# Kernel optimization log

Hardware: AMD Instinct MI355X
Metric: run time of the kernel (lower is better)

Reference implementation:

```python
import jax, jax.numpy as jnp
import numpy as np

EPS = 1e-5

def rmsnorm(x, w):
    return x * jax.lax.rsqrt(jnp.mean(x * x, axis=-1, keepdims=True) + EPS) * w

def silu(x):
    return x * jax.nn.sigmoid(x)

def causal_conv1d(x, w, b):
    # x: (B, L, D); w: (D, K) depthwise causal conv; b: (D,)
    B, L, D = x.shape
    K = w.shape[-1]
    xt = jnp.transpose(x, (0, 2, 1))  # (B, D, L)
    out = jax.lax.conv_general_dilated(
        xt, w[:, None, :], window_strides=(1,), padding=[(K - 1, 0)],
        feature_group_count=D, dimension_numbers=('NCH', 'OIH', 'NCH'))
    return jnp.transpose(out + b[None, :, None], (0, 2, 1))

def selective_scan(u, dt, A, Bm, Cm, Dp):
    # u, dt: (B,L,Di); A: (Di,S); Bm, Cm: (B,L,S); Dp: (Di,)
    dA = jnp.exp(dt[..., None] * A)                    # (B,L,Di,S)
    dBu = (dt * u)[..., None] * Bm[:, :, None, :]      # (B,L,Di,S)
    def step(h, inp):
        dA_t, dBu_t, C_t = inp
        h = dA_t * h + dBu_t
        y = jnp.einsum('bds,bs->bd', h, C_t)
        return h, y
    h0 = jnp.zeros((dA.shape[0],) + dA.shape[2:], dA.dtype)
    _, ys = jax.lax.scan(step, h0,
                         (dA.transpose(1, 0, 2, 3), dBu.transpose(1, 0, 2, 3), Cm.transpose(1, 0, 2)))
    return ys.transpose(1, 0, 2) + u * Dp

def mamba_inner(x, z, cw, cb, xpw, dpw, dpb, A_log, Dp, dt_rank, d_state):
    x = silu(causal_conv1d(x, cw, cb))
    x_dbl = jnp.einsum('bld,ed->ble', x, xpw)
    dt_r, Bm, Cm = jnp.split(x_dbl, [dt_rank, dt_rank + d_state], axis=-1)
    dt = jax.nn.softplus(jnp.einsum('blr,dr->bld', dt_r, dpw) + dpb)
    y = selective_scan(x, dt, -jnp.exp(A_log), Bm, Cm, Dp)
    return y * silu(z)

def setup_inputs() -> dict:
    key = jax.random.key(0)
    B, C, T, H, W = 2, 3, 4, 224, 224
    E, P, depth, n_spa = 384, 16, 12, 6
    Di, S, R, K = 2 * E, 8, (E + 15) // 16, 4
    N = (H // P) * (W // P)
    ks = iter(jax.random.split(key, 64))
    nrm = lambda shape, std=0.02: jax.random.normal(next(ks), shape, jnp.float32) * std
    A_init = jnp.log(jnp.tile(jnp.arange(1, S + 1, dtype=jnp.float32), (Di, 1)))
    inp = {
        'x': jax.random.normal(next(ks), (B, C, T, H, W), jnp.float32),
        'patch_w': nrm((E, C, 1, P, P)),
        'patch_b': jnp.zeros((E,), jnp.float32),
        'pos_embed': nrm((1, N, E)),
        'in_proj_w': nrm((depth, 2 * Di, E)),
        'conv_w': nrm((depth, Di, K), 0.2),
        'conv_b': jnp.zeros((depth, Di), jnp.float32),
        'xproj_w': nrm((depth, R + 2 * S, Di)),
        'dtproj_w': nrm((depth, Di, R), R ** -0.5),
        'dtproj_b': jnp.full((depth, Di), -4.0, jnp.float32) + nrm((depth, Di), 0.1),
        'A_log': jnp.tile(A_init[None], (depth, 1, 1)),
        'D_param': jnp.ones((depth, Di), jnp.float32),
        'outproj_w': nrm((depth, E, Di)),
        'norm_w': jnp.ones((depth, E), jnp.float32),
        'conv_wb': nrm((n_spa, Di, K), 0.2),
        'conv_bb': jnp.zeros((n_spa, Di), jnp.float32),
        'xproj_wb': nrm((n_spa, R + 2 * S, Di)),
        'dtproj_wb': nrm((n_spa, Di, R), R ** -0.5),
        'dtproj_bb': jnp.full((n_spa, Di), -4.0, jnp.float32) + nrm((n_spa, Di), 0.1),
        'A_log_b': jnp.tile(A_init[None], (n_spa, 1, 1)),
        'D_b': jnp.ones((n_spa, Di), jnp.float32),
        'norm_f_w': jnp.ones((E,), jnp.float32),
    }
    return inp

def reference(x, patch_w, patch_b, pos_embed, in_proj_w, conv_w, conv_b, xproj_w,
              dtproj_w, dtproj_b, A_log, D_param, outproj_w, norm_w,
              conv_wb, conv_bb, xproj_wb, dtproj_wb, dtproj_bb, A_log_b, D_b,
              norm_f_w):
    B, C, T, H, W = x.shape
    E = patch_w.shape[0]
    P = patch_w.shape[-1]
    Hp, Wp = H // P, W // P
    N = Hp * Wp
    # patch embed: Conv3d, kernel = stride = (1, P, P)
    xp = x.reshape(B, C, T, Hp, P, Wp, P)
    tok = jnp.einsum('bcthpwq,ecpq->bthwe', xp, patch_w[:, :, 0]) + patch_b
    tok = tok.reshape(B, T, N, E) + pos_embed[:, None]
    # sinusoidal temporal positional encoding
    pos = jnp.arange(T, dtype=jnp.float32)[:, None]
    div = jnp.exp(-jnp.log(10000.0) * jnp.arange(0, E, 2, dtype=jnp.float32) / E)
    pe = jnp.zeros((T, E), jnp.float32)
    pe = pe.at[:, 0::2].set(jnp.sin(pos * div)).at[:, 1::2].set(jnp.cos(pos * div))
    h = (tok + pe[None, :, None, :]).reshape(B, T * N, E)

    depth = in_proj_w.shape[0]
    n_spa = conv_wb.shape[0]
    Di = conv_w.shape[1]
    S = A_log.shape[-1]
    R = dtproj_w.shape[-1]
    residual = None
    for i in range(depth):
        residual = h if residual is None else h + residual
        hn = rmsnorm(residual, norm_w[i])
        xz = jnp.einsum('ble,fe->blf', hn, in_proj_w[i])
        xm, z = xz[..., :Di], xz[..., Di:]
        y = mamba_inner(xm, z, conv_w[i], conv_b[i], xproj_w[i],
                        dtproj_w[i], dtproj_b[i], A_log[i], D_param[i], R, S)
        if i < n_spa:  # bimamba: scan reversed sequence with backward params
            yb = mamba_inner(xm[:, ::-1], z[:, ::-1], conv_wb[i], conv_bb[i], xproj_wb[i],
                             dtproj_wb[i], dtproj_bb[i], A_log_b[i], D_b[i], R, S)
            y = y + yb[:, ::-1]
        h = jnp.einsum('bli,ei->ble', y, outproj_w[i])
    residual = h + residual
    return rmsnorm(residual, norm_f_w)
```

## Files before the change

### kernel.cpp

```cpp
#include <hip/hip_runtime.h>
#include <hip/hip_bf16.h>
#include <math.h>

#define Bn   2
#define Tn   4
#define Nn   196
#define Ln   784
#define Mn   1568
#define En   384
#define Din  768
#define Sn   8
#define Rn   24
#define DEPTH 12
#define NSPA 6
#define NC   98
#define CL   8

typedef __attribute__((ext_vector_type(8))) short bf16x8;
typedef __attribute__((ext_vector_type(4))) float f32x4;

__device__ __forceinline__ float siluf(float v) { return v / (1.f + __expf(-v)); }
__device__ __forceinline__ float us2f(unsigned short u) {
    union { unsigned int i; float f; } v; v.i = (unsigned)u << 16; return v.f;
}
__device__ __forceinline__ unsigned short f2us(float f) {
    __hip_bfloat16 b = __float2bfloat16(f);
    return *(unsigned short*)&b;
}
__device__ __forceinline__ void cstore(float* p, float v) { *p = v; }
__device__ __forceinline__ void cstore(unsigned short* p, float v) { *p = f2us(v); }

__device__ __forceinline__ void xcd_tile(int ny, int& n0, int& m0)
{
    int nx = gridDim.x;
    int total = nx*ny;
    int bid = blockIdx.y*nx + blockIdx.x;
    int q = total >> 3, r = total & 7;
    int xcd = bid & 7, idx = bid >> 3;
    int base = (xcd < r) ? xcd*(q+1) : r*(q+1) + (xcd - r)*q;
    int flat = base + idx;
    n0 = (flat / ny) * 64;
    m0 = (flat % ny) * 64;
}

#define NW0 7077888
#define NW1 3538944
#define NW2 368640
#define NW3 184320
#define NW4 294912
__device__ __forceinline__ void cast4(unsigned short* d, const float* s)
{
    float4 v = *(const float4*)s;
    ushort4 o;
    o.x = f2us(v.x); o.y = f2us(v.y); o.z = f2us(v.z); o.w = f2us(v.w);
    *(ushort4*)d = o;
}
__global__ __launch_bounds__(256) void k_castw(
    const float* __restrict__ w0, const float* __restrict__ w1,
    const float* __restrict__ w2, const float* __restrict__ w3,
    const float* __restrict__ w4,
    unsigned short* __restrict__ o0, unsigned short* __restrict__ o1,
    unsigned short* __restrict__ o2, unsigned short* __restrict__ o3,
    unsigned short* __restrict__ o4)
{
    int i4 = (blockIdx.x*blockDim.x + threadIdx.x)*4;
    if (i4 < NW0) { cast4(o0+i4, w0+i4); return; }
    i4 -= NW0;
    if (i4 < NW1) { cast4(o1+i4, w1+i4); return; }
    i4 -= NW1;
    if (i4 < NW2) { cast4(o2+i4, w2+i4); return; }
    i4 -= NW2;
    if (i4 < NW3) { cast4(o3+i4, w3+i4); return; }
    i4 -= NW3;
    if (i4 < NW4) { cast4(o4+i4, w4+i4); }
}

__global__ __launch_bounds__(256) void k_patch(
    const float* __restrict__ x, unsigned short* __restrict__ pm)
{
    int gid = blockIdx.x*blockDim.x + threadIdx.x;
    if (gid >= Mn*768) return;
    int idx = gid % 768, token = gid / 768;
    int b = token / Ln, l = token % Ln;
    int t = l / Nn, n = l % Nn;
    int hh = n / 14, ww = n % 14;
    int c = idx >> 8, rem = idx & 255, p = rem >> 4, q = rem & 15;
    pm[gid] = f2us(x[(((size_t)(b*3 + c)*Tn + t)*224 + (hh*16 + p))*224 + (ww*16 + q)]);
}

__global__ __launch_bounds__(256) void k_posadd(
    float* __restrict__ h, const float* __restrict__ pb,
    const float* __restrict__ pos)
{
    int gid = blockIdx.x*blockDim.x + threadIdx.x;
    if (gid >= Mn*En) return;
    int e = gid % En, token = gid / En;
    int l = token % Ln;
    int t = l / Nn, n = l % Nn;
    float div = __expf(-logf(10000.f) * (float)(e & ~1) / (float)En);
    float ang = (float)t * div;
    h[gid] += pb[e] + pos[n*En + e] + ((e & 1) ? cosf(ang) : sinf(ang));
}

__global__ __launch_bounds__(256) void rms_residual(
    const float* __restrict__ hin, float* __restrict__ res,
    unsigned short* __restrict__ hn, const float* __restrict__ w, int first)
{
    int wid  = (blockIdx.x * blockDim.x + threadIdx.x) >> 6;
    int lane = threadIdx.x & 63;
    if (wid >= Mn) return;
    const float* hp = hin + (size_t)wid*En;
    float* rp = res + (size_t)wid*En;
    float v[6]; float ss = 0.f;
    #pragma unroll
    for (int j = 0; j < 6; ++j) {
        int e = lane + j*64;
        float r = first ? hp[e] : (hp[e] + rp[e]);
        v[j] = r; ss = fmaf(r, r, ss);
    }
    #pragma unroll
    for (int off = 32; off; off >>= 1) ss += __shfl_xor(ss, off, 64);
    float scale = rsqrtf(ss * (1.f/(float)En) + 1e-5f);
    #pragma unroll
    for (int j = 0; j < 6; ++j) {
        int e = lane + j*64;
        rp[e] = v[j];
        hn[(size_t)wid*En + e] = f2us(v[j] * scale * w[e]);
    }
}

template<typename CT, int GATED>
__global__ __launch_bounds__(256) void gemm_mfma(
    const unsigned short* __restrict__ A,
    const unsigned short* __restrict__ Yb,
    const unsigned short* __restrict__ Z,
    const unsigned short* __restrict__ Wb,
    CT* __restrict__ C, int ldc, int M, int N, int K, int ndir)
{
    __shared__ unsigned short As[2][64][72];
    __shared__ unsigned short Bs[2][64][72];
    int n0, m0;
    xcd_tile((M + 63) >> 6, n0, m0);
    int tid = threadIdx.x;
    int wave = tid >> 6, lane = tid & 63;
    int quad = lane >> 4, fr = lane & 15;
    int arow = tid >> 2;
    int c8   = (tid & 3) << 3;
    int mg = m0 + arow; if (mg >= M) mg = M - 1;
    f32x4 acc[4] = {};

    auto gate8 = [&](const unsigned short* yf, const unsigned short* yb,
                     const unsigned short* zp) -> bf16x8 {
        bf16x8 f = *(const bf16x8*)yf;
        bf16x8 bb = *(const bf16x8*)yb;
        bf16x8 zz = *(const bf16x8*)zp;
        unsigned short o[8];
        const unsigned short* fu = (const unsigned short*)&f;
        const unsigned short* bu = (const unsigned short*)&bb;
        const unsigned short* zu = (const unsigned short*)&zz;
        #pragma unroll
        for (int j = 0; j < 8; ++j) {
            float v = us2f(fu[j]);
            if (ndir == 2) v += us2f(bu[j]);
            o[j] = f2us(v * siluf(us2f(zu[j])));
        }
        return *(bf16x8*)o;
    };

    auto load_tile = [&](int k0, bf16x8& av0, bf16x8& av1,
                         bf16x8& wv0, bf16x8& wv1) {
        if (!GATED) {
            av0 = *(const bf16x8*)(A + (size_t)mg*K + k0 + c8);
            av1 = *(const bf16x8*)(A + (size_t)mg*K + k0 + c8 + 32);
        } else {
            size_t ro = (size_t)mg*K + k0 + c8;
            size_t zo = (size_t)mg*1536 + k0 + c8;
            av0 = gate8(A + ro, Yb + ro, Z + zo);
            av1 = gate8(A + ro + 32, Yb + ro + 32, Z + zo + 32);
        }
        wv0 = *(const bf16x8*)(Wb + (size_t)(n0 + arow)*K + k0 + c8);
        wv1 = *(const bf16x8*)(Wb + (size_t)(n0 + arow)*K + k0 + c8 + 32);
    };

    {
        bf16x8 a0, a1, w0, w1;
        load_tile(0, a0, a1, w0, w1);
        *(bf16x8*)&As[0][arow][c8]      = a0;
        *(bf16x8*)&As[0][arow][c8 + 32] = a1;
        *(bf16x8*)&Bs[0][arow][c8]      = w0;
        *(bf16x8*)&Bs[0][arow][c8 + 32] = w1;
    }
    int cur = 0;
    for (int k0 = 64; k0 <= K; k0 += 64) {
        bool more = (k0 < K);
        bf16x8 a0, a1, w0, w1;
        if (more) load_tile(k0, a0, a1, w0, w1);
        __syncthreads();
        bf16x8 af0 = *(const bf16x8*)&As[cur][wave*16 + fr][quad << 3];
        bf16x8 af1 = *(const bf16x8*)&As[cur][wave*16 + fr][(quad << 3) + 32];
        #pragma unroll
        for (int nt = 0; nt < 4; ++nt) {
            bf16x8 b0 = *(const bf16x8*)&Bs[cur][nt*16 + fr][quad << 3];
            bf16x8 b1 = *(const bf16x8*)&Bs[cur][nt*16 + fr][(quad << 3) + 32];
            acc[nt] = __builtin_amdgcn_mfma_f32_16x16x32_bf16(af0, b0, acc[nt], 0, 0, 0);
            acc[nt] = __builtin_amdgcn_mfma_f32_16x16x32_bf16(af1, b1, acc[nt], 0, 0, 0);
        }
        if (more) {
            *(bf16x8*)&As[cur^1][arow][c8]      = a0;
            *(bf16x8*)&As[cur^1][arow][c8 + 32] = a1;
            *(bf16x8*)&Bs[cur^1][arow][c8]      = w0;
            *(bf16x8*)&Bs[cur^1][arow][c8 + 32] = w1;
            cur ^= 1;
        }
    }
    #pragma unroll
    for (int nt = 0; nt < 4; ++nt) {
        #pragma unroll
        for (int r = 0; r < 4; ++r) {
            int mgo = m0 + wave*16 + quad*4 + r;
            if (mgo < M) cstore(C + (size_t)mgo*ldc + n0 + nt*16 + fr, acc[nt][r]);
        }
    }
}

__global__ __launch_bounds__(256) void k_conv2(
    const unsigned short* __restrict__ xz,
    const float* __restrict__ cwf, const float* __restrict__ cbf,
    const float* __restrict__ cwb, const float* __restrict__ cbb,
    unsigned short* __restrict__ u, int ndir)
{
    int gid = blockIdx.x*blockDim.x + threadIdx.x;
    if (gid >= ndir*Mn*Din) return;
    int dir = gid / (Mn*Din);
    int rem = gid % (Mn*Din);
    int d = rem % Din, m = rem / Din;
    int l = m % Ln, b = m / Ln;
    const float* cw = dir ? cwb : cwf;
    const float* cb = dir ? cbb : cbf;
    float4 cwv = *(const float4*)(cw + d*4);
    float acc = cb[d];
    #pragma unroll
    for (int k = 0; k < 4; ++k) {
        int ls = l - 3 + k;
        if (ls < 0) continue;
        int lsrc = dir ? (Ln - 1 - ls) : ls;
        float cwk = (k==0)?cwv.x:(k==1)?cwv.y:(k==2)?cwv.z:cwv.w;
        acc = fmaf(us2f(xz[(size_t)(b*Ln + lsrc)*1536 + d]), cwk, acc);
    }
    u[gid] = f2us(siluf(acc));
}

__global__ __launch_bounds__(256) void xproj_gemm(
    const unsigned short* __restrict__ u,
    const unsigned short* __restrict__ xwf, const unsigned short* __restrict__ xwb,
    float* __restrict__ xd)
{
    __shared__ unsigned short As[2][64][72];
    __shared__ unsigned short Bs[2][64][72];
    int n0d, m0;
    xcd_tile((Mn + 63) >> 6, n0d, m0);
    int dir = n0d >> 6;
    const unsigned short* A = u + (size_t)dir*Mn*Din;
    const unsigned short* W = dir ? xwb : xwf;
    float* C = xd + (size_t)dir*Mn*40;
    int tid = threadIdx.x;
    int wave = tid >> 6, lane = tid & 63;
    int quad = lane >> 4, fr = lane & 15;
    int arow = tid >> 2;
    int c8   = (tid & 3) << 3;
    int mg = m0 + arow; if (mg >= Mn) mg = Mn - 1;
    int wrow = arow < 40 ? arow : 39;
    f32x4 acc[4] = {};

    auto load_tile = [&](int k0, bf16x8& av0, bf16x8& av1,
                         bf16x8& wv0, bf16x8& wv1) {
        av0 = *(const bf16x8*)(A + (size_t)mg*Din + k0 + c8);
        av1 = *(const bf16x8*)(A + (size_t)mg*Din + k0 + c8 + 32);
        wv0 = *(const bf16x8*)(W + (size_t)wrow*Din + k0 + c8);
        wv1 = *(const bf16x8*)(W + (size_t)wrow*Din + k0 + c8 + 32);
    };

    {
        bf16x8 a0, a1, w0, w1;
        load_tile(0, a0, a1, w0, w1);
        *(bf16x8*)&As[0][arow][c8]      = a0;
        *(bf16x8*)&As[0][arow][c8 + 32] = a1;
        *(bf16x8*)&Bs[0][arow][c8]      = w0;
        *(bf16x8*)&Bs[0][arow][c8 + 32] = w1;
    }
    int cur = 0;
    for (int k0 = 64; k0 <= Din; k0 += 64) {
        bool more = (k0 < Din);
        bf16x8 a0, a1, w0, w1;
        if (more) load_tile(k0, a0, a1, w0, w1);
        __syncthreads();
        bf16x8 af0 = *(const bf16x8*)&As[cur][wave*16 + fr][quad << 3];
        bf16x8 af1 = *(const bf16x8*)&As[cur][wave*16 + fr][(quad << 3) + 32];
        #pragma unroll
        for (int nt = 0; nt < 4; ++nt) {
            bf16x8 b0 = *(const bf16x8*)&Bs[cur][nt*16 + fr][quad << 3];
            bf16x8 b1 = *(const bf16x8*)&Bs[cur][nt*16 + fr][(quad << 3) + 32];
            acc[nt] = __builtin_amdgcn_mfma_f32_16x16x32_bf16(af0, b0, acc[nt], 0, 0, 0);
            acc[nt] = __builtin_amdgcn_mfma_f32_16x16x32_bf16(af1, b1, acc[nt], 0, 0, 0);
        }
        if (more) {
            *(bf16x8*)&As[cur^1][arow][c8]      = a0;
            *(bf16x8*)&As[cur^1][arow][c8 + 32] = a1;
            *(bf16x8*)&Bs[cur^1][arow][c8]      = w0;
            *(bf16x8*)&Bs[cur^1][arow][c8 + 32] = w1;
            cur ^= 1;
        }
    }
    #pragma unroll
    for (int nt = 0; nt < 4; ++nt) {
        int col = nt*16 + fr;
        if (col >= 40) continue;
        #pragma unroll
        for (int r = 0; r < 4; ++r) {
            int mgo = m0 + wave*16 + quad*4 + r;
            if (mgo < Mn) C[(size_t)mgo*40 + col] = acc[nt][r];
        }
    }
}

__global__ __launch_bounds__(256) void scanA(
    const unsigned short* __restrict__ u, const float* __restrict__ xd,
    const float* __restrict__ dwf, const float* __restrict__ dbf,
    const float* __restrict__ dwb, const float* __restrict__ dbb,
    const float* __restrict__ Alf, const float* __restrict__ Alb,
    float* __restrict__ Hsum, float* __restrict__ dtsum, int ndir)
{
    int gid = blockIdx.x*blockDim.x + threadIdx.x;
    if (gid >= ndir*Bn*NC*Din) return;
    int dir = gid / (Bn*NC*Din);
    int rem = gid % (Bn*NC*Din);
    int d = rem % Din;
    int bc = rem / Din;
    int c = bc % NC, b = bc / NC;
    const float* A_log = dir ? Alb : Alf;
    const float* dw = dir ? dwb : dwf;
    const float* db = dir ? dbb : dbf;
    float A[Sn];
    #pragma unroll
    for (int s = 0; s < Sn; ++s) A[s] = -__expf(A_log[d*Sn + s]);
    float dwr[Rn];
    #pragma unroll
    for (int r = 0; r < Rn; ++r) dwr[r] = dw[d*Rn + r];
    float dbv = db[d];
    float hs[Sn] = {0,0,0,0,0,0,0,0};
    float sdt = 0.f;
    int l0 = c*CL;
    const unsigned short* up = u + (size_t)dir*Mn*Din + ((size_t)b*Ln + l0)*Din + d;
    const float* xp = xd + (size_t)dir*Mn*40 + ((size_t)b*Ln + l0)*40;
    #pragma unroll
    for (int l = 0; l < CL; ++l) {
        float uv = us2f(up[(size_t)l*Din]);
        const float* xr = xp + l*40;
        float dta = dbv;
        #pragma unroll
        for (int r = 0; r < Rn; ++r) dta = fmaf(xr[r], dwr[r], dta);
        float dtv = (dta > 20.f) ? dta : log1pf(__expf(dta));
        sdt += dtv;
        const float4* B4 = (const float4*)(xr + Rn);
        float4 Bv0 = B4[0], Bv1 = B4[1];
        float du = dtv * uv;
        hs[0] = fmaf(__expf(dtv*A[0]), hs[0], du*Bv0.x);
        hs[1] = fmaf(__expf(dtv*A[1]), hs[1], du*Bv0.y);
        hs[2] = fmaf(__expf(dtv*A[2]), hs[2], du*Bv0.z);
        hs[3] = fmaf(__expf(dtv*A[3]), hs[3], du*Bv0.w);
        hs[4] = fmaf(__expf(dtv*A[4]), hs[4], du*Bv1.x);
        hs[5] = fmaf(__expf(dtv*A[5]), hs[5], du*Bv1.y);
        hs[6] = fmaf(__expf(dtv*A[6]), hs[6], du*Bv1.z);
        hs[7] = fmaf(__expf(dtv*A[7]), hs[7], du*Bv1.w);
    }
    float4* Hp = (float4*)(Hsum + (size_t)gid*8);
    Hp[0] = make_float4(hs[0], hs[1], hs[2], hs[3]);
    Hp[1] = make_float4(hs[4], hs[5], hs[6], hs[7]);
    dtsum[gid] = sdt;
}

__global__ __launch_bounds__(256) void scanB(
    const float* __restrict__ Alf, const float* __restrict__ Alb,
    float* __restrict__ Hsum, const float* __restrict__ dtsum, int ndir)
{
    int gid = blockIdx.x*blockDim.x + threadIdx.x;
    if (gid >= ndir*Bn*Din*Sn) return;
    int s   = gid & 7;
    int rem = gid >> 3;
    int d   = rem % Din;
    int t   = rem / Din;
    int b   = t % Bn, dir = t / Bn;
    const float* A_log = dir ? Alb : Alf;
    float Av = -__expf(A_log[d*Sn + s]);
    float h = 0.f;
    size_t base = (size_t)dir*Bn*NC*Din + (size_t)b*NC*Din + d;
    float* Hp = Hsum + base*8 + s;
    const float* dp = dtsum + base;
    #pragma unroll 7
    for (int c = 0; c < NC; ++c) {
        size_t off = (size_t)c*Din;
        float H = Hp[off*8];
        float sdt = dp[off];
        Hp[off*8] = h;
        h = fmaf(__expf(Av*sdt), h, H);
    }
}

__global__ __launch_bounds__(256) void scanC(
    const unsigned short* __restrict__ u, const float* __restrict__ xd,
    const float* __restrict__ dwf, const float* __restrict__ dbf,
    const float* __restrict__ dwb, const float* __restrict__ dbb,
    const float* __restrict__ Alf, const float* __restrict__ Alb,
    const float* __restrict__ Dpf, const float* __restrict__ Dpb,
    const float* __restrict__ Hsum, unsigned short* __restrict__ yt, int ndir)
{
    int gid = blockIdx.x*blockDim.x + threadIdx.x;
    if (gid >= ndir*Bn*NC*Din) return;
    int dir = gid / (Bn*NC*Din);
    int rem = gid % (Bn*NC*Din);
    int d = rem % Din;
    int bc = rem / Din;
    int c = bc % NC, b = bc / NC;
    const float* A_log = dir ? Alb : Alf;
    const float* dw = dir ? dwb : dwf;
    const float* db = dir ? dbb : dbf;
    const float* Dp = dir ? Dpb : Dpf;
    float A[Sn];
    #pragma unroll
    for (int s = 0; s < Sn; ++s) A[s] = -__expf(A_log[d*Sn + s]);
    float dwr[Rn];
    #pragma unroll
    for (int r = 0; r < Rn; ++r) dwr[r] = dw[d*Rn + r];
    float dbv = db[d];
    const float4* hp = (const float4*)(Hsum + (size_t)gid*8);
    float4 h0 = hp[0], h1 = hp[1];
    float hs[Sn] = {h0.x, h0.y, h0.z, h0.w, h1.x, h1.y, h1.z, h1.w};
    float Dd = Dp[d];
    int l0 = c*CL;
    const unsigned short* up = u + (size_t)dir*Mn*Din + ((size_t)b*Ln + l0)*Din + d;
    const float* xp = xd + (size_t)dir*Mn*40 + ((size_t)b*Ln + l0)*40;
    unsigned short* yp = yt + (size_t)dir*Mn*Din + (size_t)b*Ln*Din + d;
    #pragma unroll
    for (int l = 0; l < CL; ++l) {
        int gl = l0 + l;
        float uv = us2f(up[(size_t)l*Din]);
        const float* xr = xp + l*40;
        float dta = dbv;
        #pragma unroll
        for (int r = 0; r < Rn; ++r) dta = fmaf(xr[r], dwr[r], dta);
        float dtv = (dta > 20.f) ? dta : log1pf(__expf(dta));
        const float4* B4 = (const float4*)(xr + Rn);
        float4 Bv0 = B4[0], Bv1 = B4[1], Cv0 = B4[2], Cv1 = B4[3];
        float du = dtv * uv;
        float yv = 0.f;
        hs[0] = fmaf(__expf(dtv*A[0]), hs[0], du*Bv0.x); yv = fmaf(hs[0], Cv0.x, yv);
        hs[1] = fmaf(__expf(dtv*A[1]), hs[1], du*Bv0.y); yv = fmaf(hs[1], Cv0.y, yv);
        hs[2] = fmaf(__expf(dtv*A[2]), hs[2], du*Bv0.z); yv = fmaf(hs[2], Cv0.z, yv);
        hs[3] = fmaf(__expf(dtv*A[3]), hs[3], du*Bv0.w); yv = fmaf(hs[3], Cv0.w, yv);
        hs[4] = fmaf(__expf(dtv*A[4]), hs[4], du*Bv1.x); yv = fmaf(hs[4], Cv1.x, yv);
        hs[5] = fmaf(__expf(dtv*A[5]), hs[5], du*Bv1.y); yv = fmaf(hs[5], Cv1.y, yv);
        hs[6] = fmaf(__expf(dtv*A[6]), hs[6], du*Bv1.z); yv = fmaf(hs[6], Cv1.z, yv);
        hs[7] = fmaf(__expf(dtv*A[7]), hs[7], du*Bv1.w); yv = fmaf(hs[7], Cv1.w, yv);
        yv = fmaf(uv, Dd, yv);
        int ol = dir ? (Ln - 1 - gl) : gl;
        yp[(size_t)ol*Din] = f2us(yv);
    }
}

__global__ __launch_bounds__(256) void final_k(
    const float* __restrict__ h, const float* __restrict__ res,
    const float* __restrict__ w, float* __restrict__ out)
{
    int wid  = (blockIdx.x * blockDim.x + threadIdx.x) >> 6;
    int lane = threadIdx.x & 63;
    if (wid >= Mn) return;
    const float* hp = h + (size_t)wid*En;
    const float* rp = res + (size_t)wid*En;
    float v[6]; float ss = 0.f;
    #pragma unroll
    for (int j = 0; j < 6; ++j) {
        int e = lane + j*64;
        float r = hp[e] + rp[e];
        v[j] = r; ss = fmaf(r, r, ss);
    }
    #pragma unroll
    for (int off = 32; off; off >>= 1) ss += __shfl_xor(ss, off, 64);
    float scale = rsqrtf(ss * (1.f/(float)En) + 1e-5f);
    #pragma unroll
    for (int j = 0; j < 6; ++j) {
        int e = lane + j*64;
        out[(size_t)wid*En + e] = v[j] * scale * w[e];
    }
}

extern "C" void kernel_launch(void* const* d_in, const int* in_sizes, int n_in,
                              void* d_out, int out_size, void* d_ws, size_t ws_size,
                              hipStream_t stream)
{
    const float* x         = (const float*)d_in[0];
    const float* patch_w   = (const float*)d_in[1];
    const float* patch_b   = (const float*)d_in[2];
    const float* pos_embed = (const float*)d_in[3];
    const float* in_proj_w = (const float*)d_in[4];
    const float* conv_w    = (const float*)d_in[5];
    const float* conv_b    = (const float*)d_in[6];
    const float* xproj_w   = (const float*)d_in[7];
    const float* dtproj_w  = (const float*)d_in[8];
    const float* dtproj_b  = (const float*)d_in[9];
    const float* A_log     = (const float*)d_in[10];
    const float* D_param   = (const float*)d_in[11];
    const float* outproj_w = (const float*)d_in[12];
    const float* norm_w    = (const float*)d_in[13];
    const float* conv_wb   = (const float*)d_in[14];
    const float* conv_bb   = (const float*)d_in[15];
    const float* xproj_wb  = (const float*)d_in[16];
    const float* dtproj_wb = (const float*)d_in[17];
    const float* dtproj_bb = (const float*)d_in[18];
    const float* A_log_b   = (const float*)d_in[19];
    const float* D_b       = (const float*)d_in[20];
    const float* norm_f_w  = (const float*)d_in[21];

    float* pf   = (float*)d_ws;
    float* h    = pf;  pf += (size_t)Mn*En;
    float* res  = pf;  pf += (size_t)Mn*En;
    float* xd   = pf;  pf += (size_t)2*Mn*40;
    float* Hsum = pf;  pf += (size_t)2*Bn*NC*Din*Sn;
    float* dtsm = pf;  pf += (size_t)2*Bn*NC*Din;
    unsigned short* ub = (unsigned short*)pf;
    unsigned short* xz = ub;  ub += (size_t)Mn*1536;
    unsigned short* u  = ub;  ub += (size_t)2*Mn*Din;
    unsigned short* hn = u;
    unsigned short* yt = ub;  ub += (size_t)2*Mn*Din;
    unsigned short* w_in = ub;  ub += (size_t)NW0;
    unsigned short* w_out= ub;  ub += (size_t)NW1;
    unsigned short* w_xf = ub;  ub += (size_t)NW2;
    unsigned short* w_xb = ub;  ub += (size_t)NW3;
    unsigned short* w_pm = ub;  ub += (size_t)NW4;
    unsigned short* pm = (unsigned short*)Hsum;
    size_t needed = (size_t)((char*)ub - (char*)d_ws);
    if (ws_size < needed) return;

    const int wave_blocks = (Mn*64)/256;
    const int B_me   = (Mn*En + 255)/256;
    const int B_md   = (Mn*768 + 255)/256;
    const int B_cw   = ((NW0+NW1+NW2+NW3+NW4)/4 + 255)/256;
    const int mTiles = (Mn + 63)/64;

    k_castw<<<B_cw, 256, 0, stream>>>(in_proj_w, outproj_w, xproj_w, xproj_wb,
                                      patch_w, w_in, w_out, w_xf, w_xb, w_pm);
    k_patch<<<B_md, 256, 0, stream>>>(x, pm);
    dim3 g0(En/64, mTiles);
    gemm_mfma<float,0><<<g0, 256, 0, stream>>>(pm, nullptr, nullptr, w_pm,
                                               h, En, Mn, En, 768, 1);
    k_posadd<<<B_me, 256, 0, stream>>>(h, patch_b, pos_embed);

    for (int i = 0; i < DEPTH; ++i) {
        int ndir = (i < NSPA) ? 2 : 1;
        rms_residual<<<wave_blocks, 256, 0, stream>>>(h, res, hn, norm_w + (size_t)i*En, i == 0);

        dim3 g1(1536/64, mTiles);
        gemm_mfma<unsigned short,0><<<g1, 256, 0, stream>>>(
            hn, nullptr, nullptr, w_in + (size_t)i*1536*En,
            xz, 1536, Mn, 1536, En, 1);

        const float* cwf = conv_w + (size_t)i*Din*4;
        const float* cbf = conv_b + (size_t)i*Din;
        const float* dwf = dtproj_w + (size_t)i*Din*Rn;
        const float* dbf = dtproj_b + (size_t)i*Din;
        const float* Alf = A_log + (size_t)i*Din*Sn;
        const float* Dpf = D_param + (size_t)i*Din;
        const float* cwb = conv_wb + (size_t)i*Din*4;
        const float* cbb = conv_bb + (size_t)i*Din;
        const float* dwb = dtproj_wb + (size_t)i*Din*Rn;
        const float* dbb = dtproj_bb + (size_t)i*Din;
        const float* Alb = A_log_b + (size_t)i*Din*Sn;
        const float* Dpb = D_b + (size_t)i*Din;
        const unsigned short* xwf = w_xf + (size_t)i*40*Din;
        const unsigned short* xwb = w_xb + (size_t)i*40*Din;

        int c_blocks  = (ndir*Mn*Din + 255)/256;
        int sA_blocks = (ndir*Bn*NC*Din + 255)/256;
        int sB_blocks = (ndir*Bn*Din*Sn + 255)/256;

        k_conv2<<<c_blocks, 256, 0, stream>>>(xz, cwf, cbf, cwb, cbb, u, ndir);
        dim3 gx(ndir, mTiles);
        xproj_gemm<<<gx, 256, 0, stream>>>(u, xwf, xwb, xd);
        scanA<<<sA_blocks, 256, 0, stream>>>(u, xd, dwf, dbf, dwb, dbb,
                                             Alf, Alb, Hsum, dtsm, ndir);
        scanB<<<sB_blocks, 256, 0, stream>>>(Alf, Alb, Hsum, dtsm, ndir);
        scanC<<<sA_blocks, 256, 0, stream>>>(u, xd, dwf, dbf, dwb, dbb,
                                             Alf, Alb, Dpf, Dpb, Hsum, yt, ndir);

        dim3 g2(En/64, mTiles);
        gemm_mfma<float,1><<<g2, 256, 0, stream>>>(
            yt, yt + (size_t)Mn*Din, xz + Din, w_out + (size_t)i*En*Din,
            h, En, Mn, En, Din, ndir);
    }

    final_k<<<wave_blocks, 256, 0, stream>>>(h, res, norm_f_w, (float*)d_out);
}
```

Before: 1.261 ms.

## Split-K the narrow GEMMs into two partial buffers and fuse conv into xproj

```diff
diff --git a/kernel.cpp b/kernel.cpp
--- a/kernel.cpp
+++ b/kernel.cpp
@@ -89,8 +89,8 @@
 }
 
 __global__ __launch_bounds__(256) void k_posadd(
-    float* __restrict__ h, const float* __restrict__ pb,
-    const float* __restrict__ pos)
+    float* __restrict__ h, const float* __restrict__ h2,
+    const float* __restrict__ pb, const float* __restrict__ pos)
 {
     int gid = blockIdx.x*blockDim.x + threadIdx.x;
     if (gid >= Mn*En) return;
@@ -99,23 +99,25 @@
     int t = l / Nn, n = l % Nn;
     float div = __expf(-logf(10000.f) * (float)(e & ~1) / (float)En);
     float ang = (float)t * div;
-    h[gid] += pb[e] + pos[n*En + e] + ((e & 1) ? cosf(ang) : sinf(ang));
+    h[gid] += h2[gid] + pb[e] + pos[n*En + e] + ((e & 1) ? cosf(ang) : sinf(ang));
 }
 
 __global__ __launch_bounds__(256) void rms_residual(
-    const float* __restrict__ hin, float* __restrict__ res,
-    unsigned short* __restrict__ hn, const float* __restrict__ w, int first)
+    const float* __restrict__ hin, const float* __restrict__ h2,
+    float* __restrict__ res, unsigned short* __restrict__ hn,
+    const float* __restrict__ w, int first)
 {
     int wid  = (blockIdx.x * blockDim.x + threadIdx.x) >> 6;
     int lane = threadIdx.x & 63;
     if (wid >= Mn) return;
     const float* hp = hin + (size_t)wid*En;
+    const float* h2p = h2 + (size_t)wid*En;
     float* rp = res + (size_t)wid*En;
     float v[6]; float ss = 0.f;
     #pragma unroll
     for (int j = 0; j < 6; ++j) {
         int e = lane + j*64;
-        float r = first ? hp[e] : (hp[e] + rp[e]);
+        float r = first ? hp[e] : (hp[e] + h2p[e] + rp[e]);
         v[j] = r; ss = fmaf(r, r, ss);
     }
     #pragma unroll
@@ -129,7 +131,7 @@
     }
 }
 
-template<typename CT, int GATED>
+template<typename CT, int GATED, int SK>
 __global__ __launch_bounds__(256) void gemm_mfma(
     const unsigned short* __restrict__ A,
     const unsigned short* __restrict__ Yb,
@@ -141,6 +143,12 @@
     __shared__ unsigned short Bs[2][64][72];
     int n0, m0;
     xcd_tile((M + 63) >> 6, n0, m0);
+    int nidx = n0 >> 6;
+    int zk = nidx % SK;
+    n0 = (nidx / SK) * 64;
+    int kbeg = zk * (K / SK);
+    int kend = kbeg + K / SK;
+    CT* Cz = C + (size_t)zk*M*ldc;
     int tid = threadIdx.x;
     int wave = tid >> 6, lane = tid & 63;
     int quad = lane >> 4, fr = lane & 15;
@@ -184,15 +192,15 @@
 
     {
         bf16x8 a0, a1, w0, w1;
-        load_tile(0, a0, a1, w0, w1);
+        load_tile(kbeg, a0, a1, w0, w1);
         *(bf16x8*)&As[0][arow][c8]      = a0;
         *(bf16x8*)&As[0][arow][c8 + 32] = a1;
         *(bf16x8*)&Bs[0][arow][c8]      = w0;
         *(bf16x8*)&Bs[0][arow][c8 + 32] = w1;
     }
     int cur = 0;
-    for (int k0 = 64; k0 <= K; k0 += 64) {
-        bool more = (k0 < K);
+    for (int k0 = kbeg + 64; k0 <= kend; k0 += 64) {
+        bool more = (k0 < kend);
         bf16x8 a0, a1, w0, w1;
         if (more) load_tile(k0, a0, a1, w0, w1);
         __syncthreads();
@@ -218,50 +226,27 @@
         #pragma unroll
         for (int r = 0; r < 4; ++r) {
             int mgo = m0 + wave*16 + quad*4 + r;
-            if (mgo < M) cstore(C + (size_t)mgo*ldc + n0 + nt*16 + fr, acc[nt][r]);
-        }
-    }
-}
-
-__global__ __launch_bounds__(256) void k_conv2(
+            if (mgo < M) cstore(Cz + (size_t)mgo*ldc + n0 + nt*16 + fr, acc[nt][r]);
+        }
+    }
+}
+
+__global__ __launch_bounds__(256) void xproj_gemm(
     const unsigned short* __restrict__ xz,
     const float* __restrict__ cwf, const float* __restrict__ cbf,
     const float* __restrict__ cwb, const float* __restrict__ cbb,
-    unsigned short* __restrict__ u, int ndir)
-{
-    int gid = blockIdx.x*blockDim.x + threadIdx.x;
-    if (gid >= ndir*Mn*Din) return;
-    int dir = gid / (Mn*Din);
-    int rem = gid % (Mn*Din);
-    int d = rem % Din, m = rem / Din;
-    int l = m % Ln, b = m / Ln;
-    const float* cw = dir ? cwb : cwf;
-    const float* cb = dir ? cbb : cbf;
-    float4 cwv = *(const float4*)(cw + d*4);
-    float acc = cb[d];
-    #pragma unroll
-    for (int k = 0; k < 4; ++k) {
-        int ls = l - 3 + k;
-        if (ls < 0) continue;
-        int lsrc = dir ? (Ln - 1 - ls) : ls;
-        float cwk = (k==0)?cwv.x:(k==1)?cwv.y:(k==2)?cwv.z:cwv.w;
-        acc = fmaf(us2f(xz[(size_t)(b*Ln + lsrc)*1536 + d]), cwk, acc);
-    }
-    u[gid] = f2us(siluf(acc));
-}
-
-__global__ __launch_bounds__(256) void xproj_gemm(
-    const unsigned short* __restrict__ u,
     const unsigned short* __restrict__ xwf, const unsigned short* __restrict__ xwb,
-    float* __restrict__ xd)
+    unsigned short* __restrict__ u, float* __restrict__ xd)
 {
     __shared__ unsigned short As[2][64][72];
     __shared__ unsigned short Bs[2][64][72];
     int n0d, m0;
     xcd_tile((Mn + 63) >> 6, n0d, m0);
     int dir = n0d >> 6;
-    const unsigned short* A = u + (size_t)dir*Mn*Din;
+    const float* cw = dir ? cwb : cwf;
+    const float* cb = dir ? cbb : cbf;
     const unsigned short* W = dir ? xwb : xwf;
+    unsigned short* ud = u + (size_t)dir*Mn*Din;
     float* C = xd + (size_t)dir*Mn*40;
     int tid = threadIdx.x;
     int wave = tid >> 6, lane = tid & 63;
@@ -269,13 +254,45 @@
     int arow = tid >> 2;
     int c8   = (tid & 3) << 3;
     int mg = m0 + arow; if (mg >= Mn) mg = Mn - 1;
+    bool mvalid = (m0 + arow) < Mn;
     int wrow = arow < 40 ? arow : 39;
+    int l = mg % Ln, b = mg / Ln;
+    const unsigned short* xrow = xz + (size_t)b*Ln*1536;
     f32x4 acc[4] = {};
+
+    auto conv8 = [&](int d0) -> bf16x8 {
+        float4 cb0 = *(const float4*)(cb + d0);
+        float4 cb1 = *(const float4*)(cb + d0 + 4);
+        float av[8] = {cb0.x, cb0.y, cb0.z, cb0.w, cb1.x, cb1.y, cb1.z, cb1.w};
+        const float4* cwv = (const float4*)(cw + d0*4);
+        #pragma unroll
+        for (int k = 0; k < 4; ++k) {
+            int ls = l - 3 + k;
+            int lsrc = dir ? (Ln - 1 - ls) : ls;
+            int lsafe = (ls < 0) ? 0 : lsrc;
+            bf16x8 xv = *(const bf16x8*)(xrow + (size_t)lsafe*1536 + d0);
+            const unsigned short* xu = (const unsigned short*)&xv;
+            #pragma unroll
+            for (int j = 0; j < 8; ++j) {
+                float xf = (ls >= 0) ? us2f(xu[j]) : 0.f;
+                float wk = (k==0)?cwv[j].x:(k==1)?cwv[j].y:(k==2)?cwv[j].z:cwv[j].w;
+                av[j] = fmaf(xf, wk, av[j]);
+            }
+        }
+        unsigned short o[8];
+        #pragma unroll
+        for (int j = 0; j < 8; ++j) o[j] = f2us(siluf(av[j]));
+        return *(bf16x8*)o;
+    };
 
     auto load_tile = [&](int k0, bf16x8& av0, bf16x8& av1,
                          bf16x8& wv0, bf16x8& wv1) {
-        av0 = *(const bf16x8*)(A + (size_t)mg*Din + k0 + c8);
-        av1 = *(const bf16x8*)(A + (size_t)mg*Din + k0 + c8 + 32);
+        av0 = conv8(k0 + c8);
+        av1 = conv8(k0 + c8 + 32);
+        if (mvalid) {
+            *(bf16x8*)(ud + (size_t)mg*Din + k0 + c8)      = av0;
+            *(bf16x8*)(ud + (size_t)mg*Din + k0 + c8 + 32) = av1;
+        }
         wv0 = *(const bf16x8*)(W + (size_t)wrow*Din + k0 + c8);
         wv1 = *(const bf16x8*)(W + (size_t)wrow*Din + k0 + c8 + 32);
     };
@@ -468,19 +485,21 @@
 }
 
 __global__ __launch_bounds__(256) void final_k(
-    const float* __restrict__ h, const float* __restrict__ res,
-    const float* __restrict__ w, float* __restrict__ out)
+    const float* __restrict__ h, const float* __restrict__ h2,
+    const float* __restrict__ res, const float* __restrict__ w,
+    float* __restrict__ out)
 {
     int wid  = (blockIdx.x * blockDim.x + threadIdx.x) >> 6;
     int lane = threadIdx.x & 63;
     if (wid >= Mn) return;
     const float* hp = h + (size_t)wid*En;
+    const float* h2p = h2 + (size_t)wid*En;
     const float* rp = res + (size_t)wid*En;
     float v[6]; float ss = 0.f;
     #pragma unroll
     for (int j = 0; j < 6; ++j) {
         int e = lane + j*64;
-        float r = hp[e] + rp[e];
+        float r = hp[e] + h2p[e] + rp[e];
         v[j] = r; ss = fmaf(r, r, ss);
     }
     #pragma unroll
@@ -522,6 +541,7 @@
 
     float* pf   = (float*)d_ws;
     float* h    = pf;  pf += (size_t)Mn*En;
+    float* h2   = pf;  pf += (size_t)Mn*En;
     float* res  = pf;  pf += (size_t)Mn*En;
     float* xd   = pf;  pf += (size_t)2*Mn*40;
     float* Hsum = pf;  pf += (size_t)2*Bn*NC*Din*Sn;
@@ -549,17 +569,18 @@
     k_castw<<<B_cw, 256, 0, stream>>>(in_proj_w, outproj_w, xproj_w, xproj_wb,
                                       patch_w, w_in, w_out, w_xf, w_xb, w_pm);
     k_patch<<<B_md, 256, 0, stream>>>(x, pm);
-    dim3 g0(En/64, mTiles);
-    gemm_mfma<float,0><<<g0, 256, 0, stream>>>(pm, nullptr, nullptr, w_pm,
-                                               h, En, Mn, En, 768, 1);
-    k_posadd<<<B_me, 256, 0, stream>>>(h, patch_b, pos_embed);
+    dim3 g0((En/64)*2, mTiles);
+    gemm_mfma<float,0,2><<<g0, 256, 0, stream>>>(pm, nullptr, nullptr, w_pm,
+                                                 h, En, Mn, En, 768, 1);
+    k_posadd<<<B_me, 256, 0, stream>>>(h, h2, patch_b, pos_embed);
 
     for (int i = 0; i < DEPTH; ++i) {
         int ndir = (i < NSPA) ? 2 : 1;
-        rms_residual<<<wave_blocks, 256, 0, stream>>>(h, res, hn, norm_w + (size_t)i*En, i == 0);
+        rms_residual<<<wave_blocks, 256, 0, stream>>>(h, h2, res, hn,
+                                                      norm_w + (size_t)i*En, i == 0);
 
         dim3 g1(1536/64, mTiles);
-        gemm_mfma<unsigned short,0><<<g1, 256, 0, stream>>>(
+        gemm_mfma<unsigned short,0,1><<<g1, 256, 0, stream>>>(
             hn, nullptr, nullptr, w_in + (size_t)i*1536*En,
             xz, 1536, Mn, 1536, En, 1);
 
@@ -578,24 +599,23 @@
         const unsigned short* xwf = w_xf + (size_t)i*40*Din;
         const unsigned short* xwb = w_xb + (size_t)i*40*Din;
 
-        int c_blocks  = (ndir*Mn*Din + 255)/256;
         int sA_blocks = (ndir*Bn*NC*Din + 255)/256;
         int sB_blocks = (ndir*Bn*Din*Sn + 255)/256;
 
-        k_conv2<<<c_blocks, 256, 0, stream>>>(xz, cwf, cbf, cwb, cbb, u, ndir);
         dim3 gx(ndir, mTiles);
-        xproj_gemm<<<gx, 256, 0, stream>>>(u, xwf, xwb, xd);
+        xproj_gemm<<<gx, 256, 0, stream>>>(xz, cwf, cbf, cwb, cbb,
+                                           xwf, xwb, u, xd);
         scanA<<<sA_blocks, 256, 0, stream>>>(u, xd, dwf, dbf, dwb, dbb,
                                              Alf, Alb, Hsum, dtsm, ndir);
         scanB<<<sB_blocks, 256, 0, stream>>>(Alf, Alb, Hsum, dtsm, ndir);
         scanC<<<sA_blocks, 256, 0, stream>>>(u, xd, dwf, dbf, dwb, dbb,
                                              Alf, Alb, Dpf, Dpb, Hsum, yt, ndir);
 
-        dim3 g2(En/64, mTiles);
-        gemm_mfma<float,1><<<g2, 256, 0, stream>>>(
+        dim3 g2((En/64)*2, mTiles);
+        gemm_mfma<float,1,2><<<g2, 256, 0, stream>>>(
             yt, yt + (size_t)Mn*Din, xz + Din, w_out + (size_t)i*En*Din,
             h, En, Mn, En, Din, ndir);
     }
 
-    final_k<<<wave_blocks, 256, 0, stream>>>(h, res, norm_f_w, (float*)d_out);
-}
+    final_k<<<wave_blocks, 256, 0, stream>>>(h, h2, res, norm_f_w, (float*)d_out);
+}
```

Measured after the change: 1.424 ms. +12.9%, slower.
